# Optimization experiments

Hardware: AMD Instinct MI355X
Metric: run time of the kernel (lower is better)

## Reference

```python
import jax, jax.numpy as jnp
import numpy as np

B, S, D, H, E, K = 4, 1024, 1024, 4096, 8, 2


def setup_inputs() -> dict:
    key = jax.random.key(0)
    ks = jax.random.split(key, 5)
    std = 0.02
    return {
        "x": jax.random.normal(ks[0], (B, S, D), dtype=jnp.float32),
        "router_W": jax.random.normal(ks[1], (D, E), dtype=jnp.float32) * std,
        "W_in": jax.random.normal(ks[2], (E, D, H), dtype=jnp.float32) * std,
        "b_in": jnp.zeros((E, H), dtype=jnp.float32),
        "W_out": jax.random.normal(ks[3], (E, H, D), dtype=jnp.float32) * std,
        "b_out": jnp.zeros((E, D), dtype=jnp.float32),
    }


def reference(x, router_W, W_in, b_in, W_out, b_out):
    # ---- routing ----
    logits = jnp.einsum("bsd,de->bse", x, router_W)          # [B,S,E]
    probs = jax.nn.softmax(logits, axis=-1)                    # [B,S,E]
    top_p, top_i = jax.lax.top_k(probs, K)                     # [B,S,K]
    top_p = top_p / (jnp.sum(top_p, axis=-1, keepdims=True) + 1e-8)
    one_hot = jax.nn.one_hot(top_i, E, dtype=x.dtype)          # [B,S,K,E]
    combine = jnp.sum(one_hot * top_p[..., None], axis=-2)     # [B,S,E] per-expert weight

    # ---- experts (original runs full batch through every selected expert;
    #      with E=8, K=2 all experts are active, so run all densely) ----
    h = jnp.einsum("bsd,edh->ebsh", x, W_in) + b_in[:, None, None, :]
    h = jax.nn.gelu(h, approximate=False)
    y = jnp.einsum("ebsh,ehd->ebsd", h, W_out) + b_out[:, None, None, :]
    out = jnp.einsum("bse,ebsd->bsd", combine, y)              # weighted combine

    # ---- load-balancing aux loss ----
    expert_usage = jnp.mean(one_hot, axis=(0, 1, 2))           # f_i, fraction of routed slots
    avg_probs = jnp.mean(probs, axis=(0, 1))                   # P_i
    aux_loss = E * jnp.sum(avg_probs * expert_usage)
    return out, aux_loss
```

## Files before the change

### kernel.cpp

```cpp
#include <hip/hip_runtime.h>
#include <hip/hip_bf16.h>
#include <math.h>

#define B_ 4
#define S_ 1024
#define T_ (B_ * S_)
#define D_ 1024
#define H_ 4096
#define E_ 8
#define K_ 2
#define A_ (T_ * K_)
#define NTM_ 40

typedef __bf16 bf16x8_t __attribute__((ext_vector_type(8)));
typedef float f32x4_t __attribute__((ext_vector_type(4)));
typedef unsigned short u16x8_t __attribute__((ext_vector_type(8)));

__device__ inline unsigned short f2bf(float f) {
    __hip_bfloat16 h = __float2bfloat16(f);
    return *reinterpret_cast<unsigned short*>(&h);
}

__device__ __forceinline__ float fast_gelu(float v) {
    float z = v * 0.70710678118654752440f;
    float az = fabsf(z);
    float t = __builtin_amdgcn_rcpf(1.0f + 0.3275911f * az);
    float poly = ((((1.061405429f * t - 1.453152027f) * t + 1.421413741f) * t
                   - 0.284496736f) * t + 0.254829592f) * t;
    float e = __expf(-az * az);
    float erfv = 1.0f - poly * e;
    erfv = (z < 0.0f) ? -erfv : erfv;
    return 0.5f * v * (1.0f + erfv);
}

__device__ __forceinline__ void gl2lds16(const unsigned short* g, unsigned short* l) {
    auto* gp = reinterpret_cast<const __attribute__((address_space(1))) unsigned int*>(
        reinterpret_cast<uintptr_t>(g));
    auto* lp = reinterpret_cast<__attribute__((address_space(3))) unsigned int*>(
        reinterpret_cast<uintptr_t>(l));
    __builtin_amdgcn_global_load_lds(gp, lp, 16, 0, 0);
}

__global__ void router_kernel(const float* __restrict__ x, const float* __restrict__ rw,
                              int* __restrict__ tok_e, float* __restrict__ tok_w,
                              int* __restrict__ counts_pad, float* __restrict__ probs_pad) {
    __shared__ float s_probs[E_];
    __shared__ int s_counts[E_];
    const int tid = threadIdx.x;
    if (tid < E_) { s_probs[tid] = 0.f; s_counts[tid] = 0; }
    __syncthreads();
    const int wave = tid >> 6;
    const int lane = tid & 63;

    float wprob[E_];
    int wcount[E_];
#pragma unroll
    for (int e = 0; e < E_; ++e) { wprob[e] = 0.f; wcount[e] = 0; }

    for (int tt = 0; tt < 4; ++tt) {
        const int token = blockIdx.x * 16 + wave * 4 + tt;
        const float* xr = x + (long)token * D_;
        float acc[E_];
#pragma unroll
        for (int e = 0; e < E_; ++e) acc[e] = 0.f;
        for (int i = 0; i < D_ / 64; ++i) {
            int d = i * 64 + lane;
            float xv = xr[d];
            const float* w = rw + (long)d * E_;
#pragma unroll
            for (int e = 0; e < E_; ++e) acc[e] += xv * w[e];
        }
#pragma unroll
        for (int e = 0; e < E_; ++e) {
            for (int off = 32; off > 0; off >>= 1)
                acc[e] += __shfl_down(acc[e], off);
        }
        if (lane == 0) {
            float m = acc[0];
            for (int e = 1; e < E_; ++e) m = fmaxf(m, acc[e]);
            float p[E_], s = 0.f;
            for (int e = 0; e < E_; ++e) { p[e] = expf(acc[e] - m); s += p[e]; }
            float inv = 1.f / s;
            for (int e = 0; e < E_; ++e) { p[e] *= inv; wprob[e] += p[e]; }
            int i0 = 0;
            for (int e = 1; e < E_; ++e) if (p[e] > p[i0]) i0 = e;
            int i1 = (i0 == 0) ? 1 : 0;
            for (int e = 0; e < E_; ++e) if (e != i0 && p[e] > p[i1]) i1 = e;
            float w0 = p[i0], w1 = p[i1];
            float inv2 = 1.f / (w0 + w1 + 1e-8f);
            tok_e[token * 2] = i0;
            tok_e[token * 2 + 1] = i1;
            tok_w[token * 2] = w0 * inv2;
            tok_w[token * 2 + 1] = w1 * inv2;
            wcount[i0]++; wcount[i1]++;
        }
    }
    if (lane == 0) {
#pragma unroll
        for (int e = 0; e < E_; ++e) {
            atomicAdd(&s_probs[e], wprob[e]);
            if (wcount[e]) atomicAdd(&s_counts[e], wcount[e]);
        }
    }
    __syncthreads();
    if (tid < E_) {
        atomicAdd(&probs_pad[tid * 32], s_probs[tid]);
        if (s_counts[tid]) atomicAdd(&counts_pad[tid * 32], s_counts[tid]);
    }
}

__global__ void offsets_aux_kernel(const int* __restrict__ counts_pad,
                                   const float* __restrict__ probs_pad,
                                   int* __restrict__ offsets,
                                   int* __restrict__ tile_e, int* __restrict__ tile_m,
                                   int* __restrict__ n_tiles, float* __restrict__ aux_out) {
    if (threadIdx.x == 0 && blockIdx.x == 0) {
        int run = 0, t = 0;
        for (int e = 0; e < E_; ++e) {
            int c = counts_pad[e * 32];
            offsets[e] = run;
            for (int m0 = 0; m0 < c; m0 += 256) {
                tile_e[t] = e; tile_m[t] = m0; ++t;
            }
            run += c;
        }
        offsets[E_] = run;
        *n_tiles = t;
        float aux = 0.f;
        for (int e = 0; e < E_; ++e)
            aux += (probs_pad[e * 32] / (float)T_) * ((float)counts_pad[e * 32] / (float)A_);
        *aux_out = (float)E_ * aux;
    }
}

__global__ void scatter_kernel(const int* __restrict__ tok_e, const float* __restrict__ tok_w,
                               const int* __restrict__ offsets, int* __restrict__ cursors_pad,
                               int* __restrict__ perm_token, float* __restrict__ perm_weight,
                               int* __restrict__ inv_pos) {
    int i = blockIdx.x * blockDim.x + threadIdx.x;
    int lane = threadIdx.x & 63;
    int e = tok_e[i];
    float w = tok_w[i];
    unsigned long long bal[E_];
#pragma unroll
    for (int q = 0; q < E_; ++q) bal[q] = __ballot(e == q);
    unsigned long long below = (1ull << lane) - 1ull;
    int rank = __popcll(bal[e] & below);
    int base = 0;
    if (lane < E_) {
        int c = __popcll(bal[lane]);
        if (c) base = atomicAdd(&cursors_pad[lane * 32], c);
    }
    int mybase = __shfl(base, e);
    int pos = offsets[e] + mybase + rank;
    perm_token[pos] = i >> 1;
    perm_weight[pos] = w;
    inv_pos[i] = pos;
}

__global__ void cast_x_kernel(const float* __restrict__ x, unsigned short* __restrict__ xb) {
    long i = (long)blockIdx.x * blockDim.x + threadIdx.x;
    float4 v = reinterpret_cast<const float4*>(x)[i];
    unsigned long long packed = (unsigned long long)f2bf(v.x)
        | ((unsigned long long)f2bf(v.y) << 16)
        | ((unsigned long long)f2bf(v.z) << 32)
        | ((unsigned long long)f2bf(v.w) << 48);
    reinterpret_cast<unsigned long long*>(xb)[i] = packed;
}

__global__ void transpose_cast_kernel(const float* __restrict__ in, unsigned short* __restrict__ out,
                                      int R, int C) {
    __shared__ float tile[64][65];
    const long e = blockIdx.z;
    const float* in_e = in + e * (long)R * C;
    unsigned short* out_e = out + e * (long)R * C;
    const int c0 = blockIdx.x * 64;
    const int r0 = blockIdx.y * 64;
    const int tid = threadIdx.x;
    const int c4 = (tid & 15) * 4;
    const int rb = tid >> 4;
#pragma unroll
    for (int i = 0; i < 4; ++i) {
        const int r = rb + i * 16;
        const float4 v = *reinterpret_cast<const float4*>(&in_e[(long)(r0 + r) * C + c0 + c4]);
        tile[r][c4] = v.x; tile[r][c4 + 1] = v.y; tile[r][c4 + 2] = v.z; tile[r][c4 + 3] = v.w;
    }
    __syncthreads();
    const int rs = (tid & 7) * 8;
    const int cb = tid >> 3;
#pragma unroll
    for (int i = 0; i < 2; ++i) {
        const int c = cb + i * 32;
        u16x8_t p;
#pragma unroll
        for (int j = 0; j < 8; ++j) p[j] = f2bf(tile[rs + j][c]);
        *reinterpret_cast<u16x8_t*>(&out_e[(long)(c0 + c) * R + r0 + rs]) = p;
    }
}

template <int PHASE, int NSPLIT>
__device__ __forceinline__ void gemm_body(const unsigned short* __restrict__ A_src,
                                const unsigned short* __restrict__ B_src,
                                const float* __restrict__ bias,
                                const int* __restrict__ offsets,
                                const int* __restrict__ tile_e, const int* __restrict__ tile_m,
                                const int* __restrict__ p_ntiles,
                                const int* __restrict__ perm_token,
                                const float* __restrict__ perm_weight,
                                unsigned short* __restrict__ h_buf,
                                float* __restrict__ y_perm) {
    constexpr int Ksz  = (PHASE == 1) ? D_ : H_;
    constexpr int Kloc = Ksz / NSPLIT;
    constexpr int Nsz  = (PHASE == 1) ? H_ : D_;
    constexpr int NT   = Kloc / 32;
    constexpr int NTN  = Nsz / 256;

    const int nwg = gridDim.x;
    const int id = blockIdx.x;
    const int q = nwg >> 3, r8 = nwg & 7;
    const int xcd = id & 7, sub = id >> 3;
    const int wg = (xcd < r8 ? xcd * (q + 1) : r8 * (q + 1) + (xcd - r8) * q) + sub;
    const int mt = wg % NTM_;
    if (mt >= *p_ntiles) return;
    const int rest = wg / NTM_;
    const int nt = rest % NTN;
    const int kh = rest / NTN;
    const int e = tile_e[mt];
    const int m0 = tile_m[mt];
    const int off_e = offsets[e];
    const int n_e = offsets[e + 1] - off_e;
    const int n0 = nt * 256;
    const long k_base = (long)kh * Kloc;

    __shared__ __attribute__((aligned(16))) unsigned short lds_a[4 * 8192];
    __shared__ __attribute__((aligned(16))) unsigned short lds_b[4 * 8192];

    const int tid = threadIdx.x;
    const int lane = tid & 63;
    const int wave = tid >> 6;
    const int wr = wave >> 2;
    const int wc = wave & 3;
    const int lrow = lane & 15;
    const int kg = lane >> 4;

    const int srow = lane >> 2;
    const int grow = wave * 16 + srow;
    const int sc = (lane & 3) ^ ((grow >> 1) & 3);
    const int m_loc = m0 + grow;
    const int m_cl = (m_loc < n_e) ? m_loc : (n_e - 1);
    const int spos = off_e + m_cl;
    long arow;
    if (PHASE == 1) arow = (long)perm_token[spos] * Ksz;
    else            arow = (long)spos * Ksz;
    const unsigned short* gA = A_src + arow + k_base + sc * 8;
    const unsigned short* gB = B_src + (long)e * Nsz * Ksz + (long)(n0 + grow) * Ksz + k_base + sc * 8;
    unsigned short* const la0 = lds_a + wave * 512;
    unsigned short* const lb0 = lds_b + wave * 512;

    int aoff[4], boff[4];
#pragma unroll
    for (int i = 0; i < 4; ++i) {
        const int r = wr * 64 + i * 16 + lrow;
        aoff[i] = r * 32 + ((kg ^ ((r >> 1) & 3)) * 8);
        const int c = wc * 64 + i * 16 + lrow;
        boff[i] = c * 32 + ((kg ^ ((c >> 1) & 3)) * 8);
    }

    f32x4_t acc[4][4];
#pragma unroll
    for (int i = 0; i < 4; ++i)
#pragma unroll
        for (int j = 0; j < 4; ++j) acc[i][j] = (f32x4_t){0.f, 0.f, 0.f, 0.f};

#pragma unroll
    for (int tt = 0; tt < 3; ++tt) {
        gl2lds16(gA + tt * 32, la0 + tt * 8192);
        gl2lds16(gB + tt * 32, lb0 + tt * 8192);
    }

    for (int t = 0; t < NT; ++t) {
        if (t + 2 < NT)      asm volatile("s_waitcnt vmcnt(4)" ::: "memory");
        else if (t + 1 < NT) asm volatile("s_waitcnt vmcnt(2)" ::: "memory");
        else                 asm volatile("s_waitcnt vmcnt(0)" ::: "memory");
        __builtin_amdgcn_s_barrier();
        if (t + 3 < NT) {
            gl2lds16(gA + (t + 3) * 32, la0 + ((t + 3) & 3) * 8192);
            gl2lds16(gB + (t + 3) * 32, lb0 + ((t + 3) & 3) * 8192);
        }
        const unsigned short* la = lds_a + (t & 3) * 8192;
        const unsigned short* lb = lds_b + (t & 3) * 8192;
        bf16x8_t af[4], bf[4];
#pragma unroll
        for (int i = 0; i < 4; ++i) {
            af[i] = *reinterpret_cast<const bf16x8_t*>(la + aoff[i]);
            bf[i] = *reinterpret_cast<const bf16x8_t*>(lb + boff[i]);
        }
        asm volatile("s_waitcnt lgkmcnt(0)" ::: "memory");
        __builtin_amdgcn_sched_barrier(0);
        __builtin_amdgcn_s_setprio(1);
#pragma unroll
        for (int i = 0; i < 4; ++i)
#pragma unroll
            for (int j = 0; j < 4; ++j)
                acc[i][j] = __builtin_amdgcn_mfma_f32_16x16x32_bf16(af[i], bf[j], acc[i][j], 0, 0, 0);
        __builtin_amdgcn_s_setprio(0);
    }

    const float* bias_e = bias + (long)e * Nsz;
#pragma unroll
    for (int i = 0; i < 4; ++i) {
#pragma unroll
        for (int rq = 0; rq < 4; ++rq) {
            const int row_loc = wr * 64 + i * 16 + kg * 4 + rq;
            const int m_out = m0 + row_loc;
            if (m_out >= n_e) continue;
            const int pos = off_e + m_out;
            if (PHASE == 1) {
#pragma unroll
                for (int j = 0; j < 4; ++j) {
                    const int n = n0 + wc * 64 + j * 16 + lrow;
                    float v = acc[i][j][rq] + bias_e[n];
                    h_buf[(long)pos * Nsz + n] = f2bf(fast_gelu(v));
                }
            } else {
                float* yp = y_perm + (long)kh * ((long)A_ * D_);
                const float wgt = perm_weight[pos];
#pragma unroll
                for (int j = 0; j < 4; ++j) {
                    const int n = n0 + wc * 64 + j * 16 + lrow;
                    float v = acc[i][j][rq] + ((kh == 0) ? bias_e[n] : 0.f);
                    yp[(long)pos * Nsz + n] = v * wgt;
                }
            }
        }
    }
}

#define GEMM_ARGS const unsigned short* __restrict__ A_src, \
                  const unsigned short* __restrict__ B_src, \
                  const float* __restrict__ bias, \
                  const int* __restrict__ offsets, \
                  const int* __restrict__ tile_e, const int* __restrict__ tile_m, \
                  const int* __restrict__ p_ntiles, \
                  const int* __restrict__ perm_token, \
                  const float* __restrict__ perm_weight, \
                  unsigned short* __restrict__ h_buf, \
                  float* __restrict__ y_perm
#define GEMM_PASS A_src, B_src, bias, offsets, tile_e, tile_m, p_ntiles, \
                  perm_token, perm_weight, h_buf, y_perm

__launch_bounds__(1024, 4)
__global__ void moe_gemm_p1(GEMM_ARGS) { gemm_body<1, 1>(GEMM_PASS); }
__launch_bounds__(1024, 4)
__global__ void moe_gemm_p2s1(GEMM_ARGS) { gemm_body<2, 1>(GEMM_PASS); }
__launch_bounds__(1024, 4)
__global__ void moe_gemm_p2s2(GEMM_ARGS) { gemm_body<2, 2>(GEMM_PASS); }
__launch_bounds__(1024, 4)
__global__ void moe_gemm_p2s4(GEMM_ARGS) { gemm_body<2, 4>(GEMM_PASS); }

__global__ void combine_kernel(const float* __restrict__ y_perm, const int* __restrict__ inv_pos,
                               float* __restrict__ out, int ns) {
    int t = blockIdx.x;
    int d4 = threadIdx.x;
    int p0 = inv_pos[t * 2];
    int p1 = inv_pos[t * 2 + 1];
    float4 o = {0.f, 0.f, 0.f, 0.f};
    for (int s = 0; s < ns; ++s) {
        const float4* y = reinterpret_cast<const float4*>(y_perm + (long)s * A_ * D_);
        float4 a = y[(long)p0 * (D_ / 4) + d4];
        float4 b = y[(long)p1 * (D_ / 4) + d4];
        o.x += a.x + b.x; o.y += a.y + b.y; o.z += a.z + b.z; o.w += a.w + b.w;
    }
    reinterpret_cast<float4*>(out + (long)t * D_)[d4] = o;
}

extern "C" void kernel_launch(void* const* d_in, const int* in_sizes, int n_in,
                              void* d_out, int out_size, void* d_ws, size_t ws_size,
                              hipStream_t stream) {
    const float* x        = (const float*)d_in[0];
    const float* router_W = (const float*)d_in[1];
    const float* W_in     = (const float*)d_in[2];
    const float* b_in     = (const float*)d_in[3];
    const float* W_out    = (const float*)d_in[4];
    const float* b_out    = (const float*)d_in[5];
    float* out = (float*)d_out;

    char* ws = (char*)d_ws;
    size_t off = 0;
    auto alloc = [&](size_t bytes) -> void* {
        void* p = ws + off;
        off += (bytes + 255) & ~(size_t)255;
        return p;
    };

    int ns = 1;
    if (ws_size >= (size_t)340 * 1024 * 1024)      ns = 4;
    else if (ws_size >= (size_t)272 * 1024 * 1024) ns = 2;

    char* ctrl = (char*)alloc(4096);
    int* counts_pad   = (int*)ctrl;
    float* probs_pad  = (float*)(ctrl + 1024);
    int* cursors_pad  = (int*)(ctrl + 2048);
    int* offsets      = (int*)(ctrl + 3072);
    int* tile_e       = (int*)(ctrl + 3200);
    int* tile_m       = (int*)(ctrl + 3584);
    int* n_tiles      = (int*)(ctrl + 3968);
    int* tok_e         = (int*)alloc((size_t)A_ * 4);
    float* tok_w       = (float*)alloc((size_t)A_ * 4);
    int* perm_token    = (int*)alloc((size_t)A_ * 4);
    float* perm_weight = (float*)alloc((size_t)A_ * 4);
    int* inv_pos       = (int*)alloc((size_t)A_ * 4);
    unsigned short* x_bf    = (unsigned short*)alloc((size_t)T_ * D_ * 2);
    unsigned short* w_in_t  = (unsigned short*)alloc((size_t)E_ * D_ * H_ * 2);
    unsigned short* w_out_t = (unsigned short*)alloc((size_t)E_ * D_ * H_ * 2);
    unsigned short* h_buf   = (unsigned short*)alloc((size_t)A_ * H_ * 2);
    float* y_perm           = (float*)alloc((size_t)ns * A_ * D_ * 4);

    hipMemsetAsync(ctrl, 0, 4096, stream);

    cast_x_kernel<<<(T_ * D_ / 4) / 256, 256, 0, stream>>>(x, x_bf);
    transpose_cast_kernel<<<dim3(H_ / 64, D_ / 64, E_), 256, 0, stream>>>(W_in, w_in_t, D_, H_);
    transpose_cast_kernel<<<dim3(D_ / 64, H_ / 64, E_), 256, 0, stream>>>(W_out, w_out_t, H_, D_);
    router_kernel<<<T_ / 16, 256, 0, stream>>>(x, router_W, tok_e, tok_w, counts_pad, probs_pad);
    offsets_aux_kernel<<<1, 64, 0, stream>>>(counts_pad, probs_pad, offsets,
                                             tile_e, tile_m, n_tiles, out + (out_size - 1));
    scatter_kernel<<<A_ / 256, 256, 0, stream>>>(tok_e, tok_w, offsets, cursors_pad,
                                                 perm_token, perm_weight, inv_pos);

    moe_gemm_p1<<<NTM_ * (H_ / 256), 1024, 0, stream>>>(
        x_bf, w_in_t, b_in, offsets, tile_e, tile_m, n_tiles,
        perm_token, perm_weight, h_buf, y_perm);
    if (ns == 4) {
        moe_gemm_p2s4<<<NTM_ * (D_ / 256) * 4, 1024, 0, stream>>>(
            h_buf, w_out_t, b_out, offsets, tile_e, tile_m, n_tiles,
            perm_token, perm_weight, h_buf, y_perm);
    } else if (ns == 2) {
        moe_gemm_p2s2<<<NTM_ * (D_ / 256) * 2, 1024, 0, stream>>>(
            h_buf, w_out_t, b_out, offsets, tile_e, tile_m, n_tiles,
            perm_token, perm_weight, h_buf, y_perm);
    } else {
        moe_gemm_p2s1<<<NTM_ * (D_ / 256), 1024, 0, stream>>>(
            h_buf, w_out_t, b_out, offsets, tile_e, tile_m, n_tiles,
            perm_token, perm_weight, h_buf, y_perm);
    }
    combine_kernel<<<T_, 256, 0, stream>>>(y_perm, inv_pos, out, ns);
}
```

Before: 634.9 us.

## Fuse x bf16 cast into router, reorder GEMM LDS waits, drop split-K 4

The router kernel now reads x as float4, writes the bf16 copy of x alongside the routing logits, and the separate cast kernel is removed. That saves one full read of x and one launch. In the GEMM main loop, the lgkmcnt wait, sched_barrier and setprio are replaced by a wait placed after the MFMAs, leaving the compiler free to interleave LDS reads with MFMAs. The 4-way split of the second GEMM is removed and the 2-way split threshold is changed, which may cost parallelism when the workspace is large.

```diff
diff --git a/kernel.cpp b/kernel.cpp
--- a/kernel.cpp
+++ b/kernel.cpp
@@ -15,6 +15,7 @@
 typedef __bf16 bf16x8_t __attribute__((ext_vector_type(8)));
 typedef float f32x4_t __attribute__((ext_vector_type(4)));
 typedef unsigned short u16x8_t __attribute__((ext_vector_type(8)));
+typedef unsigned short u16x4_t __attribute__((ext_vector_type(4)));
 
 __device__ inline unsigned short f2bf(float f) {
     __hip_bfloat16 h = __float2bfloat16(f);
@@ -42,6 +43,7 @@
 }
 
 __global__ void router_kernel(const float* __restrict__ x, const float* __restrict__ rw,
+                              unsigned short* __restrict__ xb,
                               int* __restrict__ tok_e, float* __restrict__ tok_w,
                               int* __restrict__ counts_pad, float* __restrict__ probs_pad) {
     __shared__ float s_probs[E_];
@@ -60,15 +62,28 @@
     for (int tt = 0; tt < 4; ++tt) {
         const int token = blockIdx.x * 16 + wave * 4 + tt;
         const float* xr = x + (long)token * D_;
+        unsigned short* xbr = xb + (long)token * D_;
         float acc[E_];
 #pragma unroll
         for (int e = 0; e < E_; ++e) acc[e] = 0.f;
-        for (int i = 0; i < D_ / 64; ++i) {
-            int d = i * 64 + lane;
-            float xv = xr[d];
-            const float* w = rw + (long)d * E_;
-#pragma unroll
-            for (int e = 0; e < E_; ++e) acc[e] += xv * w[e];
+#pragma unroll
+        for (int i = 0; i < D_ / 256; ++i) {
+            const int d0 = i * 256 + lane * 4;
+            const float4 xv = *reinterpret_cast<const float4*>(xr + d0);
+            u16x4_t pk;
+            pk[0] = f2bf(xv.x); pk[1] = f2bf(xv.y);
+            pk[2] = f2bf(xv.z); pk[3] = f2bf(xv.w);
+            *reinterpret_cast<u16x4_t*>(xbr + d0) = pk;
+            const float xs[4] = {xv.x, xv.y, xv.z, xv.w};
+#pragma unroll
+            for (int r = 0; r < 4; ++r) {
+                const float4 w0 = *reinterpret_cast<const float4*>(rw + (long)(d0 + r) * E_);
+                const float4 w1 = *reinterpret_cast<const float4*>(rw + (long)(d0 + r) * E_ + 4);
+                acc[0] += xs[r] * w0.x; acc[1] += xs[r] * w0.y;
+                acc[2] += xs[r] * w0.z; acc[3] += xs[r] * w0.w;
+                acc[4] += xs[r] * w1.x; acc[5] += xs[r] * w1.y;
+                acc[6] += xs[r] * w1.z; acc[7] += xs[r] * w1.w;
+            }
         }
 #pragma unroll
         for (int e = 0; e < E_; ++e) {
@@ -158,16 +173,6 @@
     inv_pos[i] = pos;
 }
 
-__global__ void cast_x_kernel(const float* __restrict__ x, unsigned short* __restrict__ xb) {
-    long i = (long)blockIdx.x * blockDim.x + threadIdx.x;
-    float4 v = reinterpret_cast<const float4*>(x)[i];
-    unsigned long long packed = (unsigned long long)f2bf(v.x)
-        | ((unsigned long long)f2bf(v.y) << 16)
-        | ((unsigned long long)f2bf(v.z) << 32)
-        | ((unsigned long long)f2bf(v.w) << 48);
-    reinterpret_cast<unsigned long long*>(xb)[i] = packed;
-}
-
 __global__ void transpose_cast_kernel(const float* __restrict__ in, unsigned short* __restrict__ out,
                                       int R, int C) {
     __shared__ float tile[64][65];
@@ -283,6 +288,7 @@
         else if (t + 1 < NT) asm volatile("s_waitcnt vmcnt(2)" ::: "memory");
         else                 asm volatile("s_waitcnt vmcnt(0)" ::: "memory");
         __builtin_amdgcn_s_barrier();
+        asm volatile("" ::: "memory");
         if (t + 3 < NT) {
             gl2lds16(gA + (t + 3) * 32, la0 + ((t + 3) & 3) * 8192);
             gl2lds16(gB + (t + 3) * 32, lb0 + ((t + 3) & 3) * 8192);
@@ -295,15 +301,12 @@
             af[i] = *reinterpret_cast<const bf16x8_t*>(la + aoff[i]);
             bf[i] = *reinterpret_cast<const bf16x8_t*>(lb + boff[i]);
         }
-        asm volatile("s_waitcnt lgkmcnt(0)" ::: "memory");
-        __builtin_amdgcn_sched_barrier(0);
-        __builtin_amdgcn_s_setprio(1);
 #pragma unroll
         for (int i = 0; i < 4; ++i)
 #pragma unroll
             for (int j = 0; j < 4; ++j)
                 acc[i][j] = __builtin_amdgcn_mfma_f32_16x16x32_bf16(af[i], bf[j], acc[i][j], 0, 0, 0);
-        __builtin_amdgcn_s_setprio(0);
+        asm volatile("s_waitcnt lgkmcnt(0)" ::: "memory");
     }
 
     const float* bias_e = bias + (long)e * Nsz;
@@ -355,8 +358,6 @@
 __global__ void moe_gemm_p2s1(GEMM_ARGS) { gemm_body<2, 1>(GEMM_PASS); }
 __launch_bounds__(1024, 4)
 __global__ void moe_gemm_p2s2(GEMM_ARGS) { gemm_body<2, 2>(GEMM_PASS); }
-__launch_bounds__(1024, 4)
-__global__ void moe_gemm_p2s4(GEMM_ARGS) { gemm_body<2, 4>(GEMM_PASS); }
 
 __global__ void combine_kernel(const float* __restrict__ y_perm, const int* __restrict__ inv_pos,
                                float* __restrict__ out, int ns) {
@@ -393,9 +394,7 @@
         return p;
     };
 
-    int ns = 1;
-    if (ws_size >= (size_t)340 * 1024 * 1024)      ns = 4;
-    else if (ws_size >= (size_t)272 * 1024 * 1024) ns = 2;
+    const int ns = (ws_size >= (size_t)280 * 1024 * 1024) ? 2 : 1;
 
     char* ctrl = (char*)alloc(4096);
     int* counts_pad   = (int*)ctrl;
@@ -418,10 +417,10 @@
 
     hipMemsetAsync(ctrl, 0, 4096, stream);
 
-    cast_x_kernel<<<(T_ * D_ / 4) / 256, 256, 0, stream>>>(x, x_bf);
+    router_kernel<<<T_ / 16, 256, 0, stream>>>(x, router_W, x_bf, tok_e, tok_w,
+                                               counts_pad, probs_pad);
     transpose_cast_kernel<<<dim3(H_ / 64, D_ / 64, E_), 256, 0, stream>>>(W_in, w_in_t, D_, H_);
     transpose_cast_kernel<<<dim3(D_ / 64, H_ / 64, E_), 256, 0, stream>>>(W_out, w_out_t, H_, D_);
-    router_kernel<<<T_ / 16, 256, 0, stream>>>(x, router_W, tok_e, tok_w, counts_pad, probs_pad);
     offsets_aux_kernel<<<1, 64, 0, stream>>>(counts_pad, probs_pad, offsets,
                                              tile_e, tile_m, n_tiles, out + (out_size - 1));
     scatter_kernel<<<A_ / 256, 256, 0, stream>>>(tok_e, tok_w, offsets, cursors_pad,
@@ -430,11 +429,7 @@
     moe_gemm_p1<<<NTM_ * (H_ / 256), 1024, 0, stream>>>(
         x_bf, w_in_t, b_in, offsets, tile_e, tile_m, n_tiles,
         perm_token, perm_weight, h_buf, y_perm);
-    if (ns == 4) {
-        moe_gemm_p2s4<<<NTM_ * (D_ / 256) * 4, 1024, 0, stream>>>(
-            h_buf, w_out_t, b_out, offsets, tile_e, tile_m, n_tiles,
-            perm_token, perm_weight, h_buf, y_perm);
-    } else if (ns == 2) {
+    if (ns == 2) {
         moe_gemm_p2s2<<<NTM_ * (D_ / 256) * 2, 1024, 0, stream>>>(
             h_buf, w_out_t, b_out, offsets, tile_e, tile_m, n_tiles,
             perm_token, perm_weight, h_buf, y_perm);
```

After: 603.3 us. -5.0%, faster.
